# Kernel optimization log

Hardware: AMD Instinct MI355X
Metric: run time of the kernel (lower is better)

## Reference

```python
import jax, jax.numpy as jnp
import numpy as np


def setup_inputs() -> dict:
    key = jax.random.key(0)
    k1, k2 = jax.random.split(key)
    B, N, M, D = 2, 8192, 8192, 3
    inp = {
        "input": jax.random.normal(k1, (B, N, D), dtype=jnp.float32),
        "point": jax.random.normal(k2, (B, M, D), dtype=jnp.float32),
    }
    return inp


def reference(input, point):
    # One-sided Chamfer: for each query point, squared distance to its
    # nearest neighbor in the reference cloud `input`.
    # ||p - q||^2 = |p|^2 + |q|^2 - 2 p.q  (expanded form avoids a [B,M,N,3] tensor)
    p2 = jnp.sum(point * point, axis=-1)               # [B, M]
    q2 = jnp.sum(input * input, axis=-1)               # [B, N]
    cross = jnp.einsum("bmd,bnd->bmn", point, input)   # [B, M, N]
    d2 = p2[:, :, None] + q2[:, None, :] - 2.0 * cross
    d2 = jnp.maximum(d2, 0.0)
    return jnp.min(d2, axis=-1)                        # [B, M]
```

## Files before the change

kernel.cpp:

```cpp
#include <hip/hip_runtime.h>


typedef __attribute__((ext_vector_type(8)))  short  short8;
typedef __attribute__((ext_vector_type(16))) float  f32x16;

constexpr int BB = 2;
constexpr int NN = 8192;
constexpr int MM = 8192;

constexpr int TILES = NN / 32;
constexpr int WPB   = 8;
constexpr int TPW   = TILES / WPB;
constexpr int BQ    = WPB * 64;

__device__ inline unsigned short f2bf(float f) {
    unsigned u = __float_as_uint(f);
    return (unsigned short)((u + 0x7FFFu + ((u >> 16) & 1u)) >> 16);
}
__device__ inline float bf2f(unsigned short h) {
    return __uint_as_float((unsigned)h << 16);
}

__global__ __launch_bounds__(256) void chamfer_prep_kernel(
    const float* __restrict__ input,
    short8* __restrict__ frag)
{
    const int e = blockIdx.x * 256 + threadIdx.x;
    const int b = e >> 14;
    const int r = e & 16383;
    const int t = r >> 6, l = r & 63;
    const int n = t * 32 + (l & 31);

    const float* inb = input + (size_t)b * NN * 3;
    const float x = inb[n * 3 + 0];
    const float y = inb[n * 3 + 1];
    const float z = inb[n * 3 + 2];
    const float q2 = fmaf(z, z, fmaf(y, y, x * x));
    const unsigned short hx = f2bf(x), hy = f2bf(y), hz = f2bf(z);
    const unsigned short lx = f2bf(x - bf2f(hx));
    const unsigned short ly = f2bf(y - bf2f(hy));
    const unsigned short lz = f2bf(z - bf2f(hz));
    const unsigned short q2h = f2bf(q2);
    const unsigned short q2l = f2bf(q2 - bf2f(q2h));
    short8 v;
    if ((l >> 5) == 0) {
        v[0] = (short)hx; v[1] = (short)hy; v[2] = (short)hz; v[3] = (short)hx;
        v[4] = (short)hy; v[5] = (short)hz; v[6] = (short)lx; v[7] = (short)ly;
    } else {
        v[0] = (short)lz; v[1] = (short)q2h; v[2] = (short)q2l; v[3] = 0;
        v[4] = 0; v[5] = 0; v[6] = 0; v[7] = 0;
    }
    frag[e] = v;
}

__global__ __launch_bounds__(BQ, 4) void chamfer_main_kernel(
    const short8* __restrict__ frag,
    const float* __restrict__ point,
    float* __restrict__ out)
{
    __shared__ float pm[WPB][32];

    const int tid  = threadIdx.x;
    const int lane = tid & 63;
    const int w    = tid >> 6;
    const int b    = blockIdx.y;
    const int qb0  = blockIdx.x * 32;

    const int col = lane & 31, h = lane >> 5;
    const int m   = qb0 + col;
    const float* pp = point + ((size_t)b * MM + m) * 3;
    const float x = pp[0], y = pp[1], z = pp[2];
    const float p2 = fmaf(z, z, fmaf(y, y, x * x));
    const float hxf = bf2f(f2bf(x)), hyf = bf2f(f2bf(y)), hzf = bf2f(f2bf(z));
    const unsigned short bhx = f2bf(-2.0f * hxf);
    const unsigned short bhy = f2bf(-2.0f * hyf);
    const unsigned short bhz = f2bf(-2.0f * hzf);
    const unsigned short blx = f2bf(-2.0f * (x - hxf));
    const unsigned short bly = f2bf(-2.0f * (y - hyf));
    const unsigned short blz = f2bf(-2.0f * (z - hzf));
    const short one = (short)0x3F80;
    short8 bq;
    if (h == 0) {
        bq[0] = (short)bhx; bq[1] = (short)bhy; bq[2] = (short)bhz; bq[3] = (short)blx;
        bq[4] = (short)bly; bq[5] = (short)blz; bq[6] = (short)bhx; bq[7] = (short)bhy;
    } else {
        bq[0] = (short)bhz; bq[1] = one; bq[2] = one; bq[3] = 0;
        bq[4] = 0; bq[5] = 0; bq[6] = 0; bq[7] = 0;
    }

    f32x16 zero;
#pragma unroll
    for (int i = 0; i < 16; ++i) zero[i] = 0.0f;
    float tmin = 3.0e38f;

    const short8* fw = frag + (size_t)b * (TILES * 64) + (size_t)w * TPW * 64;
#pragma unroll 4
    for (int t = 0; t < TPW; ++t) {
        const short8 af = fw[t * 64 + lane];
        const f32x16 d = __builtin_amdgcn_mfma_f32_32x32x16_bf16(af, bq, zero, 0, 0, 0);
        const float m0 = fminf(fminf(d[0],  d[1]),  d[2]);
        const float m1 = fminf(fminf(d[3],  d[4]),  d[5]);
        const float m2 = fminf(fminf(d[6],  d[7]),  d[8]);
        const float m3 = fminf(fminf(d[9],  d[10]), d[11]);
        const float m4 = fminf(fminf(d[12], d[13]), d[14]);
        const float r0 = fminf(fminf(m0, m1), d[15]);
        const float r1 = fminf(fminf(m2, m3), m4);
        tmin = fminf(fminf(tmin, r0), r1);
    }

    tmin = fminf(tmin, __shfl_xor(tmin, 32, 64));
    if (h == 0) pm[w][col] = tmin;
    __syncthreads();
    if (w == 0 && h == 0) {
        float v = pm[0][col];
#pragma unroll
        for (int r = 1; r < WPB; ++r) v = fminf(v, pm[r][col]);
        out[(size_t)b * MM + m] = fmaxf(v + p2, 0.0f);
    }
}

extern "C" void kernel_launch(void* const* d_in, const int* in_sizes, int n_in,
                              void* d_out, int out_size, void* d_ws, size_t ws_size,
                              hipStream_t stream) {
    const float* input = (const float*)d_in[0];
    const float* point = (const float*)d_in[1];
    float* out   = (float*)d_out;
    short8* frag = (short8*)d_ws;

    chamfer_prep_kernel<<<dim3(BB * TILES * 64 / 256), dim3(256), 0, stream>>>(input, frag);

    dim3 grid(MM / 32, BB);
    chamfer_main_kernel<<<grid, dim3(BQ), 0, stream>>>(frag, point, out);
}
```

Baseline: 17.16 us.

## Stage reference fragments in LDS and split N across blocks with atomicMin

Each block now loads a slice of the reference-point fragments into shared memory once and reuses it across four waves, each handling a different group of 32 queries. Previously each wave streamed its own slice from global memory. The N dimension is split over a grid axis, and the partial minima are merged with an unsigned-integer atomicMin on the output. The prep kernel initialises the output to +inf so the atomics start from a valid value. This cuts global and L2 fragment traffic per query at the cost of an LDS fill, a block barrier, and contended atomics.

```diff
diff --git a/kernel.cpp b/kernel.cpp
--- a/kernel.cpp
+++ b/kernel.cpp
@@ -7,11 +7,13 @@
 constexpr int BB = 2;
 constexpr int NN = 8192;
 constexpr int MM = 8192;
+constexpr int BM = BB * MM;
 
 constexpr int TILES = NN / 32;
-constexpr int WPB   = 8;
-constexpr int TPW   = TILES / WPB;
-constexpr int BQ    = WPB * 64;
+constexpr int QB  = 128;
+constexpr int NS  = 8;
+constexpr int NT  = TILES / NS;
+constexpr int SE  = NT * 64;
 
 __device__ inline unsigned short f2bf(float f) {
     unsigned u = __float_as_uint(f);
@@ -23,9 +25,12 @@
 
 __global__ __launch_bounds__(256) void chamfer_prep_kernel(
     const float* __restrict__ input,
-    short8* __restrict__ frag)
+    short8* __restrict__ frag,
+    unsigned int* __restrict__ out)
 {
     const int e = blockIdx.x * 256 + threadIdx.x;
+    if (e < BM) out[e] = 0x7F800000u;
+
     const int b = e >> 14;
     const int r = e & 16383;
     const int t = r >> 6, l = r & 63;
@@ -53,21 +58,24 @@
     frag[e] = v;
 }
 
-__global__ __launch_bounds__(BQ, 4) void chamfer_main_kernel(
+__global__ __launch_bounds__(256) void chamfer_main_kernel(
     const short8* __restrict__ frag,
     const float* __restrict__ point,
-    float* __restrict__ out)
+    unsigned int* __restrict__ out)
 {
-    __shared__ float pm[WPB][32];
+    __shared__ short8 sfrag[SE];
 
     const int tid  = threadIdx.x;
     const int lane = tid & 63;
     const int w    = tid >> 6;
-    const int b    = blockIdx.y;
-    const int qb0  = blockIdx.x * 32;
+    const int b    = blockIdx.z;
+    const int qb0  = blockIdx.x * QB;
+
+    const short8* fs = frag + (size_t)b * (TILES * 64) + (size_t)blockIdx.y * SE;
+    for (int i = tid; i < SE; i += 256) sfrag[i] = fs[i];
 
     const int col = lane & 31, h = lane >> 5;
-    const int m   = qb0 + col;
+    const int m   = qb0 + w * 32 + col;
     const float* pp = point + ((size_t)b * MM + m) * 3;
     const float x = pp[0], y = pp[1], z = pp[2];
     const float p2 = fmaf(z, z, fmaf(y, y, x * x));
@@ -88,15 +96,16 @@
         bq[4] = 0; bq[5] = 0; bq[6] = 0; bq[7] = 0;
     }
 
+    __syncthreads();
+
     f32x16 zero;
 #pragma unroll
     for (int i = 0; i < 16; ++i) zero[i] = 0.0f;
     float tmin = 3.0e38f;
 
-    const short8* fw = frag + (size_t)b * (TILES * 64) + (size_t)w * TPW * 64;
 #pragma unroll 4
-    for (int t = 0; t < TPW; ++t) {
-        const short8 af = fw[t * 64 + lane];
+    for (int t = 0; t < NT; ++t) {
+        const short8 af = sfrag[t * 64 + lane];
         const f32x16 d = __builtin_amdgcn_mfma_f32_32x32x16_bf16(af, bq, zero, 0, 0, 0);
         const float m0 = fminf(fminf(d[0],  d[1]),  d[2]);
         const float m1 = fminf(fminf(d[3],  d[4]),  d[5]);
@@ -109,13 +118,9 @@
     }
 
     tmin = fminf(tmin, __shfl_xor(tmin, 32, 64));
-    if (h == 0) pm[w][col] = tmin;
-    __syncthreads();
-    if (w == 0 && h == 0) {
-        float v = pm[0][col];
-#pragma unroll
-        for (int r = 1; r < WPB; ++r) v = fminf(v, pm[r][col]);
-        out[(size_t)b * MM + m] = fmaxf(v + p2, 0.0f);
+    if (h == 0) {
+        const float d2 = fmaxf(tmin + p2, 0.0f);
+        atomicMin(out + (size_t)b * MM + m, __float_as_uint(d2));
     }
 }
 
@@ -124,11 +129,11 @@
                               hipStream_t stream) {
     const float* input = (const float*)d_in[0];
     const float* point = (const float*)d_in[1];
-    float* out   = (float*)d_out;
-    short8* frag = (short8*)d_ws;
+    unsigned int* out  = (unsigned int*)d_out;
+    short8* frag       = (short8*)d_ws;
 
-    chamfer_prep_kernel<<<dim3(BB * TILES * 64 / 256), dim3(256), 0, stream>>>(input, frag);
+    chamfer_prep_kernel<<<dim3(BB * TILES * 64 / 256), dim3(256), 0, stream>>>(input, frag, out);
 
-    dim3 grid(MM / 32, BB);
-    chamfer_main_kernel<<<grid, dim3(BQ), 0, stream>>>(frag, point, out);
+    dim3 grid(MM / QB, NS, BB);
+    chamfer_main_kernel<<<grid, dim3(256), 0, stream>>>(frag, point, out);
 }
```

Result: slower. 18.72 us (+9.1%).
